# Performance work log

Hardware: AMD Instinct MI355X
Metric: run time of the kernel (lower is better)

## Reference

```python
import jax, jax.numpy as jnp
import numpy as np

N = 100000   # num_nodes
E = 1600000  # num_edges
DIN = 128
H1 = 256
H2 = 128
SLOPE = 0.01  # torch leaky_relu default negative slope


def _gcn_conv(h, W, b, src, dst):
    # GCNConv: add self-loops, symmetric deg^-1/2 normalization, linear transform, scatter-add, bias
    hw = h @ W  # [N, out]
    loops = jnp.arange(N)
    s = jnp.concatenate([src, loops])
    d = jnp.concatenate([dst, loops])
    deg = jax.ops.segment_sum(jnp.ones(s.shape[0], dtype=hw.dtype), d, num_segments=N)
    dis = jnp.where(deg > 0, jax.lax.rsqrt(deg), 0.0)
    msg = hw[s] * (dis[s] * dis[d])[:, None]
    return jax.ops.segment_sum(msg, d, num_segments=N) + b


def _gru_cell(x, h, Wih, Whh, bih, bhh):
    # torch.nn.GRUCell semantics; weight layout [3H, in], gate order r, z, n
    gi = x @ Wih.T + bih
    gh = h @ Whh.T + bhh
    ir, iz, inn = jnp.split(gi, 3, axis=-1)
    hr, hz, hn = jnp.split(gh, 3, axis=-1)
    r = jax.nn.sigmoid(ir + hr)
    z = jax.nn.sigmoid(iz + hz)
    n = jnp.tanh(inn + r * hn)
    return (1.0 - z) * n + z * h


def setup_inputs() -> dict:
    key = jax.random.key(0)
    ks = jax.random.split(key, 24)
    rn = lambda k, shape, s=0.05: (jax.random.normal(k, shape) * s).astype(jnp.float32)
    return {
        "x": rn(ks[0], (N, DIN), 1.0),
        "edge_index": jax.random.randint(ks[1], (2, E), 0, N, dtype=jnp.int32),
        "prev0": rn(ks[2], (N, H1), 1.0),
        "prev1": rn(ks[3], (N, H2), 1.0),
        "Wp1": rn(ks[4], (DIN, 256)), "bp1": jnp.zeros((256,), jnp.float32),
        "Wp2": rn(ks[5], (256, 128)), "bp2": jnp.zeros((128,), jnp.float32),
        "Wc1": rn(ks[6], (128, H1)), "bc1": jnp.zeros((H1,), jnp.float32),
        "Wc2": rn(ks[7], (H1, H2)), "bc2": jnp.zeros((H2,), jnp.float32),
        "Wih1": rn(ks[8], (3 * H1, H1)), "Whh1": rn(ks[9], (3 * H1, H1)),
        "bih1": jnp.zeros((3 * H1,), jnp.float32), "bhh1": jnp.zeros((3 * H1,), jnp.float32),
        "Wih2": rn(ks[10], (3 * H2, H2)), "Whh2": rn(ks[11], (3 * H2, H2)),
        "bih2": jnp.zeros((3 * H2,), jnp.float32), "bhh2": jnp.zeros((3 * H2,), jnp.float32),
        "Wpost": rn(ks[12], (H2, 2)), "bpost": jnp.zeros((2,), jnp.float32),
    }


def reference(x, edge_index, prev0, prev1, Wp1, bp1, Wp2, bp2, Wc1, bc1, Wc2, bc2,
              Wih1, Whh1, bih1, bhh1, Wih2, Whh2, bih2, bhh2, Wpost, bpost):
    src, dst = edge_index[0], edge_index[1]
    # preprocess MLP (dropout p=0 => identity)
    h = jax.nn.leaky_relu(x @ Wp1 + bp1, SLOPE)
    h = jax.nn.leaky_relu(h @ Wp2 + bp2, SLOPE)
    # GCN layer 1 + GRU temporal update
    h = jax.nn.leaky_relu(_gcn_conv(h, Wc1, bc1, src, dst), SLOPE)
    h = _gru_cell(h, prev0, Wih1, Whh1, bih1, bhh1)
    emb0 = h
    # GCN layer 2 + GRU temporal update
    h = jax.nn.leaky_relu(_gcn_conv(h, Wc2, bc2, src, dst), SLOPE)
    h = _gru_cell(h, prev1, Wih2, Whh2, bih2, bhh2)
    emb1 = h
    # postprocess and reduce
    out = jnp.sum(h @ Wpost + bpost, axis=-1)  # [N]
    return out, emb0, emb1
```

## Files before the change

kernel.cpp:

```cpp
#include <hip/hip_runtime.h>
#include <cstdint>
#include <cstddef>

typedef __bf16 bf16x8 __attribute__((ext_vector_type(8)));
typedef float f32x4 __attribute__((ext_vector_type(4)));
typedef unsigned short us16;

__device__ __forceinline__ float lrelu(float v) { return v >= 0.0f ? v : 0.01f * v; }
__device__ __forceinline__ float fsigmoid(float x) {
  x = fminf(fmaxf(x, -30.0f), 30.0f);
  return 1.0f / (1.0f + __expf(-x));
}
__device__ __forceinline__ float ftanh(float x) {
  x = fminf(fmaxf(x, -15.0f), 15.0f);
  float e = __expf(2.0f * x);
  return (e - 1.0f) / (e + 1.0f);
}
__device__ __forceinline__ us16 f2b(float f) {
  unsigned int u = __builtin_bit_cast(unsigned int, f);
  u = (u + 0x7fffu + ((u >> 16) & 1u)) >> 16;
  return (us16)u;
}
__device__ __forceinline__ float b2f(us16 h) {
  unsigned int u = ((unsigned int)h) << 16;
  return __builtin_bit_cast(float, u);
}
__device__ __forceinline__ unsigned pk2(float a, float b) {
  return (unsigned)f2b(a) | ((unsigned)f2b(b) << 16);
}
__device__ __forceinline__ void unp8(int4 v, float* t) {
  unsigned a = (unsigned)v.x, b = (unsigned)v.y, c = (unsigned)v.z, d = (unsigned)v.w;
  t[0] = b2f((us16)(a & 0xffff)); t[1] = b2f((us16)(a >> 16));
  t[2] = b2f((us16)(b & 0xffff)); t[3] = b2f((us16)(b >> 16));
  t[4] = b2f((us16)(c & 0xffff)); t[5] = b2f((us16)(c >> 16));
  t[6] = b2f((us16)(d & 0xffff)); t[7] = b2f((us16)(d >> 16));
}

__device__ __forceinline__ void stage16(const us16* gsrc, us16* ldst) {
  __builtin_amdgcn_global_load_lds(
      (const __attribute__((address_space(1))) unsigned int*)(const void*)gsrc,
      (__attribute__((address_space(3))) unsigned int*)(void*)ldst, 16, 0, 0);
}
__device__ __forceinline__ bf16x8 frag_rd(const us16* base, int row, int byte_in_row) {
  int byte = row * 128 + (byte_in_row ^ ((row & 7) << 4));
  return *(const bf16x8*)((const char*)base + byte);
}
__device__ __forceinline__ bf16x8 frd32(const us16* tilebase, int row, int ck16) {
  int slot = ck16 ^ ((row >> 1) & 3);
  return *(const bf16x8*)(tilebase + row * 32 + slot * 8);
}

__global__ void k_deg(const int* __restrict__ dst, int* __restrict__ indeg, int E) {
  int e = blockIdx.x * 256 + threadIdx.x;
  if (e < E) atomicAdd(&indeg[dst[e]], 1);
}

__global__ void k_dis(const int* __restrict__ indeg, float* __restrict__ dis, int n) {
  int i = blockIdx.x * 256 + threadIdx.x;
  if (i < n) dis[i] = rsqrtf((float)(indeg[i] + 1));
}

__global__ __launch_bounds__(1024) void k_scan1(const int* __restrict__ v, int* __restrict__ rp,
                                                int* __restrict__ part, int n) {
  __shared__ int wsum[16];
  int base = blockIdx.x << 10;
  int t = threadIdx.x, lane = t & 63, wv = t >> 6;
  int val = (base + t < n) ? v[base + t] : 0;
  int s = val;
  #pragma unroll
  for (int off = 1; off < 64; off <<= 1) {
    int u = __shfl_up(s, off);
    if (lane >= off) s += u;
  }
  if (lane == 63) wsum[wv] = s;
  __syncthreads();
  int wadd = 0;
  #pragma unroll
  for (int w = 0; w < 16; ++w) wadd += (w < wv) ? wsum[w] : 0;
  if (base + t < n) rp[base + t] = wadd + s - val;
  if (t == 0) {
    int tot = 0;
    #pragma unroll
    for (int w = 0; w < 16; ++w) tot += wsum[w];
    part[blockIdx.x] = tot;
  }
}

__global__ __launch_bounds__(1024) void k_scan2(int* __restrict__ p, int nc) {
  __shared__ int wsum[16];
  int t = threadIdx.x, lane = t & 63, wv = t >> 6;
  int val = (t < nc) ? p[t] : 0;
  int s = val;
  #pragma unroll
  for (int off = 1; off < 64; off <<= 1) {
    int u = __shfl_up(s, off);
    if (lane >= off) s += u;
  }
  if (lane == 63) wsum[wv] = s;
  __syncthreads();
  int wadd = 0;
  #pragma unroll
  for (int w = 0; w < 16; ++w) wadd += (w < wv) ? wsum[w] : 0;
  if (t < nc) p[t] = wadd + s - val;
}

__global__ void k_scan3(int* __restrict__ rp, const int* __restrict__ part, int n, int total) {
  int i = blockIdx.x * 256 + threadIdx.x;
  if (i < n) rp[i] += part[i >> 10];
  else if (i == n) rp[n] = total;
}

__global__ void k_fill(const int* __restrict__ src, const int* __restrict__ dst,
                       const float* __restrict__ dis, int* __restrict__ cursor,
                       int* __restrict__ csrc, float* __restrict__ cw, int E) {
  int e = blockIdx.x * 256 + threadIdx.x;
  if (e >= E) return;
  int s = src[e], d = dst[e];
  int pos = atomicAdd(&cursor[d], 1);
  csrc[pos] = s;
  cw[pos] = dis[s] * dis[d];
}

__global__ void k_cast(const float* __restrict__ in, us16* __restrict__ out, int n) {
  int i = (blockIdx.x * 256 + threadIdx.x) * 4;
  if (i >= n) return;
  float4 v = *(const float4*)(in + i);
  *(ushort4*)(out + i) = make_ushort4(f2b(v.x), f2b(v.y), f2b(v.z), f2b(v.w));
}

__global__ void k_tpose(const float* __restrict__ in, us16* __restrict__ out, int R, int C) {
  int t = blockIdx.x * 256 + threadIdx.x;
  if (t >= R * C) return;
  int r = t % R, c = t / R;
  out[(size_t)c * R + r] = f2b(in[(size_t)r * C + c]);
}

template<int ACT, int BIAS>
__global__ __launch_bounds__(256) void k_mm(const us16* __restrict__ A,
                                            const us16* __restrict__ Bt,
                                            const float* __restrict__ bias,
                                            us16* __restrict__ Cb,
                                            int M, int K, int Nc, int ny) {
  __shared__ __align__(16) us16 lds[2][2 * 8192];
  const int bm = (blockIdx.x / ny) * 128;
  const int bn = (blockIdx.x % ny) * 128;
  const int tid = threadIdx.x;
  const int lane = tid & 63;
  const int wave = tid >> 6;
  const int wm = (wave >> 1) * 64;
  const int wn = (wave & 1) * 64;
  const int lr = lane & 15;
  const int lk = lane >> 4;
  const int srow = lane >> 3;
  const int schk = (lane & 7) ^ srow;
  f32x4 acc[4][4] = {};

  auto stage = [&](int k0, us16* buf) {
    #pragma unroll
    for (int it = 0; it < 4; ++it) {
      int r8 = (wave * 4 + it) * 8;
      int ar = bm + r8 + srow; if (ar >= M) ar = M - 1;
      stage16(A + (size_t)ar * K + k0 + schk * 8, buf + r8 * 64);
      stage16(Bt + (size_t)(bn + r8 + srow) * K + k0 + schk * 8, buf + 8192 + r8 * 64);
    }
  };

  const int nk = K >> 6;
  stage(0, lds[0]);
  for (int t = 0; t < nk; ++t) {
    us16* cur = lds[t & 1];
    __syncthreads();
    if (t + 1 < nk) stage((t + 1) << 6, lds[(t + 1) & 1]);
    #pragma unroll
    for (int kk = 0; kk < 2; ++kk) {
      bf16x8 af[4], bq[4];
      #pragma unroll
      for (int i = 0; i < 4; ++i) af[i] = frag_rd(cur, wm + i * 16 + lr, kk * 64 + lk * 16);
      #pragma unroll
      for (int j = 0; j < 4; ++j) bq[j] = frag_rd(cur + 8192, wn + j * 16 + lr, kk * 64 + lk * 16);
      #pragma unroll
      for (int i = 0; i < 4; ++i)
        #pragma unroll
        for (int j = 0; j < 4; ++j)
          acc[i][j] = __builtin_amdgcn_mfma_f32_16x16x32_bf16(af[i], bq[j], acc[i][j], 0, 0, 0);
    }
  }
  float bb[4];
  #pragma unroll
  for (int j = 0; j < 4; ++j) bb[j] = BIAS ? bias[bn + wn + j * 16 + lr] : 0.0f;
  #pragma unroll
  for (int i = 0; i < 4; ++i) {
    #pragma unroll
    for (int q = 0; q < 4; ++q) {
      int row = bm + wm + i * 16 + lk * 4 + q;
      if (row < M) {
        #pragma unroll
        for (int j = 0; j < 4; ++j) {
          int col = bn + wn + j * 16 + lr;
          float v = acc[i][j][q] + bb[j];
          if (ACT) v = lrelu(v);
          Cb[(size_t)row * Nc + col] = f2b(v);
        }
      }
    }
  }
}

template<int ACT>
__global__ __launch_bounds__(256) void k_agg128(const us16* __restrict__ hw, const int* __restrict__ rp,
                                                const int* __restrict__ csrc, const float* __restrict__ cw,
                                                const float* __restrict__ dis, const float* __restrict__ bias,
                                                us16* __restrict__ outp, int M) {
  int node = blockIdx.x * 16 + (threadIdx.x >> 4);
  int l = threadIdx.x & 15;
  if (node >= M) return;
  const us16* base = hw + l * 8;
  float acc[8], t0[8], t1[8], t2[8], t3[8];
  float dn = dis[node];
  float sw = dn * dn;
  {
    int4 v = *(const int4*)(base + (size_t)node * 128);
    unp8(v, t0);
    #pragma unroll
    for (int j = 0; j < 8; ++j) acc[j] = t0[j] * sw;
  }
  int e = rp[node], e1 = rp[node + 1];
  for (; e + 4 <= e1; e += 4) {
    int s0 = csrc[e], s1 = csrc[e + 1], s2 = csrc[e + 2], s3 = csrc[e + 3];
    float w0 = cw[e], w1 = cw[e + 1], w2 = cw[e + 2], w3 = cw[e + 3];
    int4 v0 = *(const int4*)(base + (size_t)s0 * 128);
    int4 v1 = *(const int4*)(base + (size_t)s1 * 128);
    int4 v2 = *(const int4*)(base + (size_t)s2 * 128);
    int4 v3 = *(const int4*)(base + (size_t)s3 * 128);
    unp8(v0, t0); unp8(v1, t1); unp8(v2, t2); unp8(v3, t3);
    #pragma unroll
    for (int j = 0; j < 8; ++j) acc[j] = fmaf(w0, t0[j], acc[j]);
    #pragma unroll
    for (int j = 0; j < 8; ++j) acc[j] = fmaf(w1, t1[j], acc[j]);
    #pragma unroll
    for (int j = 0; j < 8; ++j) acc[j] = fmaf(w2, t2[j], acc[j]);
    #pragma unroll
    for (int j = 0; j < 8; ++j) acc[j] = fmaf(w3, t3[j], acc[j]);
  }
  for (; e < e1; ++e) {
    int s0 = csrc[e];
    float w0 = cw[e];
    int4 v0 = *(const int4*)(base + (size_t)s0 * 128);
    unp8(v0, t0);
    #pragma unroll
    for (int j = 0; j < 8; ++j) acc[j] = fmaf(w0, t0[j], acc[j]);
  }
  if (ACT) {
    float4 b0 = *(const float4*)(bias + l * 8);
    float4 b1 = *(const float4*)(bias + l * 8 + 4);
    float bb[8] = {b0.x, b0.y, b0.z, b0.w, b1.x, b1.y, b1.z, b1.w};
    #pragma unroll
    for (int j = 0; j < 8; ++j) acc[j] = lrelu(acc[j] + bb[j]);
  }
  int4 o;
  o.x = (int)pk2(acc[0], acc[1]);
  o.y = (int)pk2(acc[2], acc[3]);
  o.z = (int)pk2(acc[4], acc[5]);
  o.w = (int)pk2(acc[6], acc[7]);
  *(int4*)(outp + (size_t)node * 128 + l * 8) = o;
}

template<int H, int WB>
__global__ __launch_bounds__(256) void k_fgru(const us16* __restrict__ xb, const us16* __restrict__ hb,
                                              const us16* __restrict__ Wih, const us16* __restrict__ Whh,
                                              const float* __restrict__ bih, const float* __restrict__ bhh,
                                              float* __restrict__ emb, us16* __restrict__ embb,
                                              int M, int ny) {
  __shared__ __align__(16) us16 lds[2][8 * 2048];
  const int bn = (blockIdx.x % ny) * 64;
  const int bm = (blockIdx.x / ny) * 64;
  const int tid = threadIdx.x;
  const int lane = tid & 63, wave = tid >> 6;
  const int wm = (wave >> 1) * 32, wn = (wave & 1) * 32;
  const int lr = lane & 15, lk = lane >> 4;
  const int sl_row = lane >> 2;
  const int sl_chk = (lane & 3) ^ ((lane >> 3) & 3);

  f32x4 acc[6][2][2];
  #pragma unroll
  for (int g = 0; g < 6; ++g)
    #pragma unroll
    for (int i = 0; i < 2; ++i)
      #pragma unroll
      for (int j = 0; j < 2; ++j) acc[g][i][j] = {0.f, 0.f, 0.f, 0.f};

  auto stage_step = [&](int k0, us16* buf) {
    #pragma unroll
    for (int it = 0; it < 8; ++it) {
      int m = wave * 8 + it;
      int t = m >> 2, q = m & 3;
      int r0 = q * 16;
      int lrow = r0 + sl_row;
      const us16* src;
      if (t == 0) {
        int ar = bm + lrow; if (ar >= M) ar = M - 1;
        src = xb + (size_t)ar * H + k0 + sl_chk * 8;
      } else if (t == 1) {
        int ar = bm + lrow; if (ar >= M) ar = M - 1;
        src = hb + (size_t)ar * H + k0 + sl_chk * 8;
      } else {
        int w = t - 2;
        const us16* W = (w < 3) ? Wih : Whh;
        int g = (w < 3) ? w : w - 3;
        src = W + (size_t)(g * H + bn + lrow) * H + k0 + sl_chk * 8;
      }
      stage16(src, buf + t * 2048 + r0 * 32);
    }
  };

  const int nk = H >> 5;
  stage_step(0, lds[0]);
  for (int t = 0; t < nk; ++t) {
    us16* cur = lds[t & 1];
    __syncthreads();
    if (t + 1 < nk) stage_step((t + 1) << 5, lds[(t + 1) & 1]);
    bf16x8 ax[2], ah[2];
    #pragma unroll
    for (int i = 0; i < 2; ++i) {
      ax[i] = frd32(cur, wm + i * 16 + lr, lk);
      ah[i] = frd32(cur + 2048, wm + i * 16 + lr, lk);
    }
    #pragma unroll
    for (int g = 0; g < 3; ++g) {
      bf16x8 bqi[2], bqh[2];
      #pragma unroll
      for (int j = 0; j < 2; ++j) {
        bqi[j] = frd32(cur + (2 + g) * 2048, wn + j * 16 + lr, lk);
        bqh[j] = frd32(cur + (5 + g) * 2048, wn + j * 16 + lr, lk);
      }
      #pragma unroll
      for (int i = 0; i < 2; ++i)
        #pragma unroll
        for (int j = 0; j < 2; ++j) {
          acc[g][i][j] = __builtin_amdgcn_mfma_f32_16x16x32_bf16(ax[i], bqi[j], acc[g][i][j], 0, 0, 0);
          acc[3 + g][i][j] = __builtin_amdgcn_mfma_f32_16x16x32_bf16(ah[i], bqh[j], acc[3 + g][i][j], 0, 0, 0);
        }
    }
  }
  #pragma unroll
  for (int j = 0; j < 2; ++j) {
    int col = bn + wn + j * 16 + lr;
    float bir = bih[col], biz = bih[H + col], bin = bih[2 * H + col];
    float bhr = bhh[col], bhz = bhh[H + col], bhn = bhh[2 * H + col];
    #pragma unroll
    for (int i = 0; i < 2; ++i) {
      #pragma unroll
      for (int q = 0; q < 4; ++q) {
        int row = bm + wm + i * 16 + lk * 4 + q;
        if (row >= M) continue;
        float r = fsigmoid(acc[0][i][j][q] + bir + acc[3][i][j][q] + bhr);
        float z = fsigmoid(acc[1][i][j][q] + biz + acc[4][i][j][q] + bhz);
        float n = ftanh(acc[2][i][j][q] + bin + r * (acc[5][i][j][q] + bhn));
        float hv = b2f(hb[(size_t)row * H + col]);
        float o = (1.0f - z) * n + z * hv;
        emb[(size_t)row * H + col] = o;
        if (WB) embb[(size_t)row * H + col] = f2b(o);
      }
    }
  }
}

__global__ __launch_bounds__(256) void k_post(const float* __restrict__ emb, const float* __restrict__ Wpost,
                                              const float* __restrict__ bpost, float* __restrict__ outv, int M) {
  int gw = (int)((blockIdx.x * 256 + threadIdx.x) >> 6);
  int lane = threadIdx.x & 63;
  if (gw >= M) return;
  float2 ev = *(const float2*)(emb + (size_t)gw * 128 + lane * 2);
  float4 wv = *(const float4*)(Wpost + lane * 4);
  float p = ev.x * (wv.x + wv.y) + ev.y * (wv.z + wv.w);
  #pragma unroll
  for (int o = 32; o > 0; o >>= 1) p += __shfl_xor(p, o);
  if (lane == 0) outv[gw] = p + bpost[0] + bpost[1];
}

extern "C" void kernel_launch(void* const* d_in, const int* in_sizes, int n_in,
                              void* d_out, int out_size, void* d_ws, size_t ws_size,
                              hipStream_t stream) {
  const float* x     = (const float*)d_in[0];
  const int*   ei    = (const int*)d_in[1];
  const float* prev0 = (const float*)d_in[2];
  const float* prev1 = (const float*)d_in[3];
  const float* Wp1   = (const float*)d_in[4];
  const float* bp1   = (const float*)d_in[5];
  const float* Wp2   = (const float*)d_in[6];
  const float* bp2   = (const float*)d_in[7];
  const float* Wc1   = (const float*)d_in[8];
  const float* bc1   = (const float*)d_in[9];
  const float* Wc2   = (const float*)d_in[10];
  const float* bc2   = (const float*)d_in[11];
  const float* Wih1  = (const float*)d_in[12];
  const float* Whh1  = (const float*)d_in[13];
  const float* bih1  = (const float*)d_in[14];
  const float* bhh1  = (const float*)d_in[15];
  const float* Wih2  = (const float*)d_in[16];
  const float* Whh2  = (const float*)d_in[17];
  const float* bih2  = (const float*)d_in[18];
  const float* bhh2  = (const float*)d_in[19];
  const float* Wpost = (const float*)d_in[20];
  const float* bpost = (const float*)d_in[21];

  const int N = in_sizes[0] / 128;
  const int E = in_sizes[1] / 2;
  const int* srcp = ei;
  const int* dstp = ei + E;

  char* wsb = (char*)d_ws;
  size_t off = 0;
  auto alloc = [&](size_t bytes) -> void* {
    void* p = wsb + off;
    off = (off + bytes + 255) & ~(size_t)255;
    return p;
  };
  float* dis    = (float*)alloc((size_t)N * 4);
  int*   indeg  = (int*)alloc((size_t)N * 4);
  int*   rp     = (int*)alloc((size_t)(N + 1) * 4);
  int*   part   = (int*)alloc((size_t)1024 * 4);
  int*   cursor = (int*)alloc((size_t)N * 4);
  int*   csrc   = (int*)alloc((size_t)E * 4);
  float* cw     = (float*)alloc((size_t)E * 4);
  us16* xb    = (us16*)alloc((size_t)N * 128 * 2);
  us16* p0b   = (us16*)alloc((size_t)N * 256 * 2);
  us16* p1b   = (us16*)alloc((size_t)N * 128 * 2);
  us16* WtP1  = (us16*)alloc((size_t)256 * 128 * 2);
  us16* WtP2  = (us16*)alloc((size_t)128 * 256 * 2);
  us16* WtC1  = (us16*)alloc((size_t)256 * 128 * 2);
  us16* WtC2  = (us16*)alloc((size_t)128 * 256 * 2);
  us16* Wih1b = (us16*)alloc((size_t)768 * 256 * 2);
  us16* Whh1b = (us16*)alloc((size_t)768 * 256 * 2);
  us16* Wih2b = (us16*)alloc((size_t)384 * 128 * 2);
  us16* Whh2b = (us16*)alloc((size_t)384 * 128 * 2);
  us16* bufA  = (us16*)alloc((size_t)N * 256 * 2);
  us16* bufB  = (us16*)alloc((size_t)N * 128 * 2);
  us16* bufD  = (us16*)alloc((size_t)N * 128 * 2);
  us16* emb0b = (us16*)alloc((size_t)N * 256 * 2);
  (void)ws_size; (void)n_in; (void)out_size;

  float* outv = (float*)d_out;
  float* emb0 = outv + N;
  float* emb1 = emb0 + (size_t)N * 256;

  auto cg = [](long n) { return (unsigned)((n / 4 + 255) / 256); };

  k_cast<<<cg((long)N * 128), 256, 0, stream>>>(x, xb, N * 128);
  k_cast<<<cg((long)N * 256), 256, 0, stream>>>(prev0, p0b, N * 256);
  k_cast<<<cg((long)N * 128), 256, 0, stream>>>(prev1, p1b, N * 128);
  k_cast<<<cg(768 * 256), 256, 0, stream>>>(Wih1, Wih1b, 768 * 256);
  k_cast<<<cg(768 * 256), 256, 0, stream>>>(Whh1, Whh1b, 768 * 256);
  k_cast<<<cg(384 * 128), 256, 0, stream>>>(Wih2, Wih2b, 384 * 128);
  k_cast<<<cg(384 * 128), 256, 0, stream>>>(Whh2, Whh2b, 384 * 128);
  k_tpose<<<(128 * 256 + 255) / 256, 256, 0, stream>>>(Wp1, WtP1, 128, 256);
  k_tpose<<<(256 * 128 + 255) / 256, 256, 0, stream>>>(Wp2, WtP2, 256, 128);
  k_tpose<<<(128 * 256 + 255) / 256, 256, 0, stream>>>(Wc1, WtC1, 128, 256);
  k_tpose<<<(256 * 128 + 255) / 256, 256, 0, stream>>>(Wc2, WtC2, 256, 128);

  hipMemsetAsync(indeg, 0, (size_t)N * 4, stream);
  k_deg<<<(E + 255) / 256, 256, 0, stream>>>(dstp, indeg, E);
  k_dis<<<(N + 255) / 256, 256, 0, stream>>>(indeg, dis, N);
  const int NC = (N + 1023) / 1024;
  k_scan1<<<NC, 1024, 0, stream>>>(indeg, rp, part, N);
  k_scan2<<<1, 1024, 0, stream>>>(part, NC);
  k_scan3<<<(N + 256) / 256, 256, 0, stream>>>(rp, part, N, E);
  hipMemcpyAsync(cursor, rp, (size_t)N * 4, hipMemcpyDeviceToDevice, stream);
  k_fill<<<(E + 255) / 256, 256, 0, stream>>>(srcp, dstp, dis, cursor, csrc, cw, E);

  const int MB = (N + 127) / 128;
  const int FB = (N + 63) / 64;
  const int AB = (N + 15) / 16;

  k_mm<1, 1><<<MB * 2, 256, 0, stream>>>(xb, WtP1, bp1, bufA, N, 128, 256, 2);
  k_mm<1, 1><<<MB, 256, 0, stream>>>(bufA, WtP2, bp2, bufB, N, 256, 128, 1);
  k_agg128<0><<<AB, 256, 0, stream>>>(bufB, rp, csrc, cw, dis, nullptr, bufD, N);
  k_mm<1, 1><<<MB * 2, 256, 0, stream>>>(bufD, WtC1, bc1, bufA, N, 128, 256, 2);
  k_fgru<256, 1><<<FB * 4, 256, 0, stream>>>(bufA, p0b, Wih1b, Whh1b, bih1, bhh1,
                                             emb0, emb0b, N, 4);
  k_mm<0, 0><<<MB, 256, 0, stream>>>(emb0b, WtC2, nullptr, bufB, N, 256, 128, 1);
  k_agg128<1><<<AB, 256, 0, stream>>>(bufB, rp, csrc, cw, dis, bc2, bufD, N);
  k_fgru<128, 0><<<FB * 2, 256, 0, stream>>>(bufD, p1b, Wih2b, Whh2b, bih2, bhh2,
                                             emb1, nullptr, N, 2);
  k_post<<<(N + 3) / 4, 256, 0, stream>>>(emb1, Wpost, bpost, outv, N);
}
```

Baseline: 799.9 us.

## Restructure GRU kernel into split-role waves, fuse postprocess and prep kernels

The fused GRU kernel now uses 512-thread blocks with 128x32 tiles. Paired waves compute the input-side and hidden-side gate products separately, then exchange partial results through LDS. Workgroups are remapped across 8 XCDs, and the final Wpost reduction is folded into the second GRU epilogue using atomics into a zeroed output. Separately, the weight cast and transpose kernels merge into one launch, dis is computed inside scan1, and scan3 writes the cursor so the device-to-device memcpy goes away. The aim is fewer launches, less emb1 rereading and better locality, at the cost of atomics and an LDS exchange with extra syncs.

```diff
diff --git a/kernel.cpp b/kernel.cpp
--- a/kernel.cpp
+++ b/kernel.cpp
@@ -55,17 +55,13 @@
   if (e < E) atomicAdd(&indeg[dst[e]], 1);
 }
 
-__global__ void k_dis(const int* __restrict__ indeg, float* __restrict__ dis, int n) {
-  int i = blockIdx.x * 256 + threadIdx.x;
-  if (i < n) dis[i] = rsqrtf((float)(indeg[i] + 1));
-}
-
 __global__ __launch_bounds__(1024) void k_scan1(const int* __restrict__ v, int* __restrict__ rp,
-                                                int* __restrict__ part, int n) {
+                                                int* __restrict__ part, float* __restrict__ dis, int n) {
   __shared__ int wsum[16];
   int base = blockIdx.x << 10;
   int t = threadIdx.x, lane = t & 63, wv = t >> 6;
   int val = (base + t < n) ? v[base + t] : 0;
+  if (base + t < n) dis[base + t] = rsqrtf((float)(val + 1));
   int s = val;
   #pragma unroll
   for (int off = 1; off < 64; off <<= 1) {
@@ -104,10 +100,16 @@
   if (t < nc) p[t] = wadd + s - val;
 }
 
-__global__ void k_scan3(int* __restrict__ rp, const int* __restrict__ part, int n, int total) {
+__global__ void k_scan3(int* __restrict__ rp, const int* __restrict__ part,
+                        int* __restrict__ cursor, int n, int total) {
   int i = blockIdx.x * 256 + threadIdx.x;
-  if (i < n) rp[i] += part[i >> 10];
-  else if (i == n) rp[n] = total;
+  if (i < n) {
+    int v = rp[i] + part[i >> 10];
+    rp[i] = v;
+    cursor[i] = v;
+  } else if (i == n) {
+    rp[n] = total;
+  }
 }
 
 __global__ void k_fill(const int* __restrict__ src, const int* __restrict__ dst,
@@ -128,11 +130,30 @@
   *(ushort4*)(out + i) = make_ushort4(f2b(v.x), f2b(v.y), f2b(v.z), f2b(v.w));
 }
 
-__global__ void k_tpose(const float* __restrict__ in, us16* __restrict__ out, int R, int C) {
-  int t = blockIdx.x * 256 + threadIdx.x;
-  if (t >= R * C) return;
-  int r = t % R, c = t / R;
-  out[(size_t)c * R + r] = f2b(in[(size_t)r * C + c]);
+__global__ void k_prepw(const float* __restrict__ Wih1, const float* __restrict__ Whh1,
+                        const float* __restrict__ Wih2, const float* __restrict__ Whh2,
+                        const float* __restrict__ Wp1, const float* __restrict__ Wp2,
+                        const float* __restrict__ Wc1, const float* __restrict__ Wc2,
+                        us16* __restrict__ Wih1b, us16* __restrict__ Whh1b,
+                        us16* __restrict__ Wih2b, us16* __restrict__ Whh2b,
+                        us16* __restrict__ WtP1, us16* __restrict__ WtP2,
+                        us16* __restrict__ WtC1, us16* __restrict__ WtC2) {
+  int e = blockIdx.x * 256 + threadIdx.x;
+  if (e < 196608) { Wih1b[e] = f2b(Wih1[e]); return; }
+  e -= 196608;
+  if (e < 196608) { Whh1b[e] = f2b(Whh1[e]); return; }
+  e -= 196608;
+  if (e < 49152) { Wih2b[e] = f2b(Wih2[e]); return; }
+  e -= 49152;
+  if (e < 49152) { Whh2b[e] = f2b(Whh2[e]); return; }
+  e -= 49152;
+  if (e < 32768) { int r = e & 127, c = e >> 7; WtP1[e] = f2b(Wp1[(size_t)r * 256 + c]); return; }
+  e -= 32768;
+  if (e < 32768) { int r = e & 255, c = e >> 8; WtP2[e] = f2b(Wp2[(size_t)r * 128 + c]); return; }
+  e -= 32768;
+  if (e < 32768) { int r = e & 127, c = e >> 7; WtC1[e] = f2b(Wc1[(size_t)r * 256 + c]); return; }
+  e -= 32768;
+  if (e < 32768) { int r = e & 255, c = e >> 8; WtC2[e] = f2b(Wc2[(size_t)r * 128 + c]); }
 }
 
 template<int ACT, int BIAS>
@@ -265,51 +286,56 @@
   *(int4*)(outp + (size_t)node * 128 + l * 8) = o;
 }
 
-template<int H, int WB>
-__global__ __launch_bounds__(256) void k_fgru(const us16* __restrict__ xb, const us16* __restrict__ hb,
+template<int H, int WB, int PH>
+__global__ __launch_bounds__(512) void k_fgru(const us16* __restrict__ xb, const us16* __restrict__ hb,
                                               const us16* __restrict__ Wih, const us16* __restrict__ Whh,
                                               const float* __restrict__ bih, const float* __restrict__ bhh,
                                               float* __restrict__ emb, us16* __restrict__ embb,
-                                              int M, int ny) {
-  __shared__ __align__(16) us16 lds[2][8 * 2048];
-  const int bn = (blockIdx.x % ny) * 64;
-  const int bm = (blockIdx.x / ny) * 64;
+                                              const float* __restrict__ Wpost, const float* __restrict__ bpost,
+                                              float* __restrict__ outv, int M, int ny) {
+  __shared__ __align__(16) us16 lds[2][14336];
+  const int nwg = gridDim.x;
+  int bid = blockIdx.x;
+  {
+    int q8 = nwg >> 3, r8 = nwg & 7;
+    int xc = bid & 7, ix = bid >> 3;
+    bid = (xc < r8 ? xc * (q8 + 1) : r8 * (q8 + 1) + (xc - r8) * q8) + ix;
+  }
+  const int bn = (bid % ny) * 32;
+  const int bm = (bid / ny) * 128;
   const int tid = threadIdx.x;
   const int lane = tid & 63, wave = tid >> 6;
-  const int wm = (wave >> 1) * 32, wn = (wave & 1) * 32;
+  const int pair = wave >> 1;
+  const int role = wave & 1;
+  const int wm = pair * 32;
   const int lr = lane & 15, lk = lane >> 4;
   const int sl_row = lane >> 2;
   const int sl_chk = (lane & 3) ^ ((lane >> 3) & 3);
 
-  f32x4 acc[6][2][2];
-  #pragma unroll
-  for (int g = 0; g < 6; ++g)
-    #pragma unroll
-    for (int i = 0; i < 2; ++i)
-      #pragma unroll
-      for (int j = 0; j < 2; ++j) acc[g][i][j] = {0.f, 0.f, 0.f, 0.f};
+  f32x4 acc[3][2][2] = {};
 
   auto stage_step = [&](int k0, us16* buf) {
     #pragma unroll
-    for (int it = 0; it < 8; ++it) {
-      int m = wave * 8 + it;
-      int t = m >> 2, q = m & 3;
-      int r0 = q * 16;
-      int lrow = r0 + sl_row;
+    for (int it = 0; it < 4; ++it) {
+      int m = wave * 4 + it;
+      if (m >= 28) break;
       const us16* src;
-      if (t == 0) {
-        int ar = bm + lrow; if (ar >= M) ar = M - 1;
-        src = xb + (size_t)ar * H + k0 + sl_chk * 8;
-      } else if (t == 1) {
-        int ar = bm + lrow; if (ar >= M) ar = M - 1;
-        src = hb + (size_t)ar * H + k0 + sl_chk * 8;
+      us16* dst;
+      if (m < 16) {
+        int r0 = (m & 7) * 16;
+        int ar = bm + r0 + sl_row; if (ar >= M) ar = M - 1;
+        src = (m < 8 ? xb : hb) + (size_t)ar * H + k0 + sl_chk * 8;
+        dst = buf + (m < 8 ? 0 : 4096) + r0 * 32;
       } else {
-        int w = t - 2;
-        const us16* W = (w < 3) ? Wih : Whh;
-        int g = (w < 3) ? w : w - 3;
-        src = W + (size_t)(g * H + bn + lrow) * H + k0 + sl_chk * 8;
+        int wi = m - 16;
+        int g6 = wi >> 1;
+        int r0 = (wi & 1) * 16;
+        const us16* W = (g6 < 3) ? Wih : Whh;
+        int gg = (g6 < 3) ? g6 : g6 - 3;
+        src = W + (size_t)(gg * H + bn + r0 + sl_row) * H + k0 + sl_chk * 8;
+        dst = buf + 8192 + g6 * 1024 + r0 * 32;
       }
-      stage16(src, buf + t * 2048 + r0 * 32);
+      stage16(src, dst);
     }
   };
 
@@ -319,63 +345,77 @@
     us16* cur = lds[t & 1];
     __syncthreads();
     if (t + 1 < nk) stage_step((t + 1) << 5, lds[(t + 1) & 1]);
-    bf16x8 ax[2], ah[2];
-    #pragma unroll
-    for (int i = 0; i < 2; ++i) {
-      ax[i] = frd32(cur, wm + i * 16 + lr, lk);
-      ah[i] = frd32(cur + 2048, wm + i * 16 + lr, lk);
-    }
+    const us16* at = cur + (role ? 4096 : 0);
+    bf16x8 a0 = frd32(at, wm + lr, lk);
+    bf16x8 a1 = frd32(at, wm + 16 + lr, lk);
     #pragma unroll
     for (int g = 0; g < 3; ++g) {
-      bf16x8 bqi[2], bqh[2];
-      #pragma unroll
-      for (int j = 0; j < 2; ++j) {
-        bqi[j] = frd32(cur + (2 + g) * 2048, wn + j * 16 + lr, lk);
-        bqh[j] = frd32(cur + (5 + g) * 2048, wn + j * 16 + lr, lk);
-      }
+      const us16* wt = cur + 8192 + (role * 3 + g) * 1024;
+      bf16x8 b0 = frd32(wt, lr, lk);
+      bf16x8 b1 = frd32(wt, 16 + lr, lk);
+      acc[g][0][0] = __builtin_amdgcn_mfma_f32_16x16x32_bf16(a0, b0, acc[g][0][0], 0, 0, 0);
+      acc[g][0][1] = __builtin_amdgcn_mfma_f32_16x16x32_bf16(a0, b1, acc[g][0][1], 0, 0, 0);
+      acc[g][1][0] = __builtin_amdgcn_mfma_f32_16x16x32_bf16(a1, b0, acc[g][1][0], 0, 0, 0);
+      acc[g][1][1] = __builtin_amdgcn_mfma_f32_16x16x32_bf16(a1, b1, acc[g][1][1], 0, 0, 0);
+    }
+  }
+  __syncthreads();
+  float* xch = (float*)&lds[0][0];
+  if (role) {
+    #pragma unroll
+    for (int g = 0; g < 3; ++g)
       #pragma unroll
       for (int i = 0; i < 2; ++i)
         #pragma unroll
-        for (int j = 0; j < 2; ++j) {
-          acc[g][i][j] = __builtin_amdgcn_mfma_f32_16x16x32_bf16(ax[i], bqi[j], acc[g][i][j], 0, 0, 0);
-          acc[3 + g][i][j] = __builtin_amdgcn_mfma_f32_16x16x32_bf16(ah[i], bqh[j], acc[3 + g][i][j], 0, 0, 0);
+        for (int j = 0; j < 2; ++j)
+          *(f32x4*)&xch[((((pair * 3 + g) * 2 + i) * 2 + j) * 64 + lane) * 4] = acc[g][i][j];
+  }
+  __syncthreads();
+  if (!role) {
+    float part[2][4] = {};
+    #pragma unroll
+    for (int j = 0; j < 2; ++j) {
+      int col = bn + j * 16 + lr;
+      float bir = bih[col], biz = bih[H + col], bin = bih[2 * H + col];
+      float bhr = bhh[col], bhz = bhh[H + col], bhn = bhh[2 * H + col];
+      float wps = 0.0f;
+      if (PH) wps = Wpost[2 * col] + Wpost[2 * col + 1];
+      #pragma unroll
+      for (int i = 0; i < 2; ++i) {
+        f32x4 gr_ = *(const f32x4*)&xch[((((pair * 3 + 0) * 2 + i) * 2 + j) * 64 + lane) * 4];
+        f32x4 gz_ = *(const f32x4*)&xch[((((pair * 3 + 1) * 2 + i) * 2 + j) * 64 + lane) * 4];
+        f32x4 gn_ = *(const f32x4*)&xch[((((pair * 3 + 2) * 2 + i) * 2 + j) * 64 + lane) * 4];
+        #pragma unroll
+        for (int q = 0; q < 4; ++q) {
+          int row = bm + wm + i * 16 + lk * 4 + q;
+          if (row < M) {
+            float r = fsigmoid(acc[0][i][j][q] + bir + gr_[q] + bhr);
+            float z = fsigmoid(acc[1][i][j][q] + biz + gz_[q] + bhz);
+            float n = ftanh(acc[2][i][j][q] + bin + r * (gn_[q] + bhn));
+            float hv = b2f(hb[(size_t)row * H + col]);
+            float o = (1.0f - z) * n + z * hv;
+            emb[(size_t)row * H + col] = o;
+            if (WB) embb[(size_t)row * H + col] = f2b(o);
+            if (PH) part[i][q] += o * wps;
+          }
         }
-    }
-  }
-  #pragma unroll
-  for (int j = 0; j < 2; ++j) {
-    int col = bn + wn + j * 16 + lr;
-    float bir = bih[col], biz = bih[H + col], bin = bih[2 * H + col];
-    float bhr = bhh[col], bhz = bhh[H + col], bhn = bhh[2 * H + col];
-    #pragma unroll
-    for (int i = 0; i < 2; ++i) {
+      }
+    }
+    if (PH) {
+      float bsum = bpost[0] + bpost[1];
       #pragma unroll
-      for (int q = 0; q < 4; ++q) {
-        int row = bm + wm + i * 16 + lk * 4 + q;
-        if (row >= M) continue;
-        float r = fsigmoid(acc[0][i][j][q] + bir + acc[3][i][j][q] + bhr);
-        float z = fsigmoid(acc[1][i][j][q] + biz + acc[4][i][j][q] + bhz);
-        float n = ftanh(acc[2][i][j][q] + bin + r * (acc[5][i][j][q] + bhn));
-        float hv = b2f(hb[(size_t)row * H + col]);
-        float o = (1.0f - z) * n + z * hv;
-        emb[(size_t)row * H + col] = o;
-        if (WB) embb[(size_t)row * H + col] = f2b(o);
-      }
-    }
-  }
-}
-
-__global__ __launch_bounds__(256) void k_post(const float* __restrict__ emb, const float* __restrict__ Wpost,
-                                              const float* __restrict__ bpost, float* __restrict__ outv, int M) {
-  int gw = (int)((blockIdx.x * 256 + threadIdx.x) >> 6);
-  int lane = threadIdx.x & 63;
-  if (gw >= M) return;
-  float2 ev = *(const float2*)(emb + (size_t)gw * 128 + lane * 2);
-  float4 wv = *(const float4*)(Wpost + lane * 4);
-  float p = ev.x * (wv.x + wv.y) + ev.y * (wv.z + wv.w);
-  #pragma unroll
-  for (int o = 32; o > 0; o >>= 1) p += __shfl_xor(p, o);
-  if (lane == 0) outv[gw] = p + bpost[0] + bpost[1];
+      for (int i = 0; i < 2; ++i)
+        #pragma unroll
+        for (int q = 0; q < 4; ++q) {
+          float v = part[i][q];
+          v += __shfl_xor(v, 1); v += __shfl_xor(v, 2);
+          v += __shfl_xor(v, 4); v += __shfl_xor(v, 8);
+          int row = bm + wm + i * 16 + lk * 4 + q;
+          if (lr == 0 && row < M)
+            atomicAdd(&outv[row], v + (bn == 0 ? bsum : 0.0f));
+        }
+    }
+  }
 }
 
 extern "C" void kernel_launch(void* const* d_in, const int* in_sizes, int n_in,
@@ -446,41 +486,33 @@
 
   auto cg = [](long n) { return (unsigned)((n / 4 + 255) / 256); };
 
+  hipMemsetAsync(outv, 0, (size_t)N * 4, stream);
+
   k_cast<<<cg((long)N * 128), 256, 0, stream>>>(x, xb, N * 128);
   k_cast<<<cg((long)N * 256), 256, 0, stream>>>(prev0, p0b, N * 256);
   k_cast<<<cg((long)N * 128), 256, 0, stream>>>(prev1, p1b, N * 128);
-  k_cast<<<cg(768 * 256), 256, 0, stream>>>(Wih1, Wih1b, 768 * 256);
-  k_cast<<<cg(768 * 256), 256, 0, stream>>>(Whh1, Whh1b, 768 * 256);
-  k_cast<<<cg(384 * 128), 256, 0, stream>>>(Wih2, Wih2b, 384 * 128);
-  k_cast<<<cg(384 * 128), 256, 0, stream>>>(Whh2, Whh2b, 384 * 128);
-  k_tpose<<<(128 * 256 + 255) / 256, 256, 0, stream>>>(Wp1, WtP1, 128, 256);
-  k_tpose<<<(256 * 128 + 255) / 256, 256, 0, stream>>>(Wp2, WtP2, 256, 128);
-  k_tpose<<<(128 * 256 + 255) / 256, 256, 0, stream>>>(Wc1, WtC1, 128, 256);
-  k_tpose<<<(256 * 128 + 255) / 256, 256, 0, stream>>>(Wc2, WtC2, 256, 128);
+  k_prepw<<<2432, 256, 0, stream>>>(Wih1, Whh1, Wih2, Whh2, Wp1, Wp2, Wc1, Wc2,
+                                    Wih1b, Whh1b, Wih2b, Whh2b, WtP1, WtP2, WtC1, WtC2);
 
   hipMemsetAsync(indeg, 0, (size_t)N * 4, stream);
   k_deg<<<(E + 255) / 256, 256, 0, stream>>>(dstp, indeg, E);
-  k_dis<<<(N + 255) / 256, 256, 0, stream>>>(indeg, dis, N);
   const int NC = (N + 1023) / 1024;
-  k_scan1<<<NC, 1024, 0, stream>>>(indeg, rp, part, N);
+  k_scan1<<<NC, 1024, 0, stream>>>(indeg, rp, part, dis, N);
   k_scan2<<<1, 1024, 0, stream>>>(part, NC);
-  k_scan3<<<(N + 256) / 256, 256, 0, stream>>>(rp, part, N, E);
-  hipMemcpyAsync(cursor, rp, (size_t)N * 4, hipMemcpyDeviceToDevice, stream);
+  k_scan3<<<(N + 256) / 256, 256, 0, stream>>>(rp, part, cursor, N, E);
   k_fill<<<(E + 255) / 256, 256, 0, stream>>>(srcp, dstp, dis, cursor, csrc, cw, E);
 
   const int MB = (N + 127) / 128;
-  const int FB = (N + 63) / 64;
   const int AB = (N + 15) / 16;
 
   k_mm<1, 1><<<MB * 2, 256, 0, stream>>>(xb, WtP1, bp1, bufA, N, 128, 256, 2);
   k_mm<1, 1><<<MB, 256, 0, stream>>>(bufA, WtP2, bp2, bufB, N, 256, 128, 1);
   k_agg128<0><<<AB, 256, 0, stream>>>(bufB, rp, csrc, cw, dis, nullptr, bufD, N);
   k_mm<1, 1><<<MB * 2, 256, 0, stream>>>(bufD, WtC1, bc1, bufA, N, 128, 256, 2);
-  k_fgru<256, 1><<<FB * 4, 256, 0, stream>>>(bufA, p0b, Wih1b, Whh1b, bih1, bhh1,
-                                             emb0, emb0b, N, 4);
+  k_fgru<256, 1, 0><<<MB * 8, 512, 0, stream>>>(bufA, p0b, Wih1b, Whh1b, bih1, bhh1,
+                                                emb0, emb0b, nullptr, nullptr, nullptr, N, 8);
   k_mm<0, 0><<<MB, 256, 0, stream>>>(emb0b, WtC2, nullptr, bufB, N, 256, 128, 1);
   k_agg128<1><<<AB, 256, 0, stream>>>(bufB, rp, csrc, cw, dis, bc2, bufD, N);
-  k_fgru<128, 0><<<FB * 2, 256, 0, stream>>>(bufD, p1b, Wih2b, Whh2b, bih2, bhh2,
-                                             emb1, nullptr, N, 2);
-  k_post<<<(N + 3) / 4, 256, 0, stream>>>(emb1, Wpost, bpost, outv, N);
-}
+  k_fgru<128, 0, 1><<<MB * 4, 512, 0, stream>>>(bufD, p1b, Wih2b, Whh2b, bih2, bhh2,
+                                                emb1, nullptr, Wpost, bpost, outv, N, 4);
+}
```

Result: no change. 803.1 us (+0.4%).
